# Kernel optimization log

Measured on AMD Instinct MI355X. Metric: run time of the kernel, lower is better.

The kernel has to match this reference:

```python
import jax, jax.numpy as jnp
import numpy as np

N_NODES = 100000
N_EDGES = 1600000
N_GRAPHS = 128
DIM = 128
N_LAYERS = 4
EPS = 1e-5


def setup_inputs() -> dict:
    key = jax.random.key(0)
    ks = jax.random.split(key, 8)
    h = jax.random.normal(ks[0], (N_NODES, DIM), dtype=jnp.float32)
    src = jax.random.randint(ks[1], (N_EDGES,), 0, N_NODES, dtype=jnp.int32)
    dst = jax.random.randint(ks[2], (N_EDGES,), 0, N_NODES, dtype=jnp.int32)
    graph_id = jnp.sort(jax.random.randint(ks[3], (N_NODES,), 0, N_GRAPHS, dtype=jnp.int32))
    sc = 1.0 / np.sqrt(DIM)
    W_embed = jax.random.normal(ks[4], (DIM, DIM), dtype=jnp.float32) * sc
    b_embed = jnp.zeros((DIM,), jnp.float32)
    W_layers = jax.random.normal(ks[5], (N_LAYERS, DIM, DIM), dtype=jnp.float32) * sc
    b_layers = jnp.zeros((N_LAYERS, DIM), jnp.float32)
    gamma = jnp.ones((N_LAYERS, DIM), jnp.float32)
    beta = jnp.zeros((N_LAYERS, DIM), jnp.float32)
    return {"h": h, "src": src, "dst": dst, "graph_id": graph_id,
            "W_embed": W_embed, "b_embed": b_embed, "W_layers": W_layers,
            "b_layers": b_layers, "gamma": gamma, "beta": beta}


def _gcn_forward(h, src, dst, graph_id, W_embed, b_embed, W_layers, b_layers, gamma, beta):
    # symmetric GraphConv normalization (norm='both'): D_out^{-1/2} on src, D_in^{-1/2} on dst
    ones_e = jnp.ones((src.shape[0],), h.dtype)
    deg_out = jax.ops.segment_sum(ones_e, src, num_segments=N_NODES)
    deg_in = jax.ops.segment_sum(ones_e, dst, num_segments=N_NODES)
    norm_src = jax.lax.rsqrt(jnp.maximum(deg_out, 1.0))
    norm_dst = jax.lax.rsqrt(jnp.maximum(deg_in, 1.0))

    # input embedding (dropout = identity in eval)
    h = h @ W_embed + b_embed

    for l in range(N_LAYERS):
        h_in = h
        # gather-aggregate-scatter: m_e = h_src * norm_src; sum into dst; scale by norm_dst
        m = (h * norm_src[:, None])[src]                         # [E, D]
        agg = jax.ops.segment_sum(m, dst, num_segments=N_NODES)  # [N, D]
        hl = (agg * norm_dst[:, None]) @ W_layers[l] + b_layers[l]
        # batch norm over node dimension (training-mode batch stats)
        mu = jnp.mean(hl, axis=0)
        var = jnp.var(hl, axis=0)
        hl = (hl - mu) * jax.lax.rsqrt(var + EPS) * gamma[l] + beta[l]
        hl = jax.nn.relu(hl)
        h = hl + h_in  # residual (dims match all layers)

    # mean readout per graph
    sums = jax.ops.segment_sum(h, graph_id, num_segments=N_GRAPHS)           # [G, D]
    cnts = jax.ops.segment_sum(jnp.ones((N_NODES,), h.dtype), graph_id, num_segments=N_GRAPHS)
    return sums / jnp.maximum(cnts, 1.0)[:, None]


def reference(h, src, dst, graph_id, W_embed, b_embed, W_layers, b_layers, gamma, beta):
    return _gcn_forward(h, src, dst, graph_id, W_embed, b_embed, W_layers, b_layers, gamma, beta)
```

## Files before the change

kernel.cpp:

```cpp
#include <hip/hip_runtime.h>
#include <hip/hip_bf16.h>
#include <hip/hip_fp16.h>


#define N_NODES 100000
#define N_EDGES 1600000
#define N_GRAPHS 128
#define DIM 128
#define N_LAYERS 4
#define BN_EPS 1e-5f
#define NBUCK 196
#define EPB 6250
#define SREP 64

typedef __attribute__((ext_vector_type(8))) _Float16 half8;
typedef __attribute__((ext_vector_type(4))) float floatx4;
typedef __attribute__((ext_vector_type(2))) float floatx2;

__global__ __launch_bounds__(256) void binA_k(const int* __restrict__ src,
                                              const int* __restrict__ dst,
                                              int* __restrict__ cnt_d,
                                              int* __restrict__ cnt_s,
                                              int* __restrict__ bh_d,
                                              int* __restrict__ bh_s) {
  __shared__ int hd[NBUCK], hs[NBUCK];
  int t = threadIdx.x;
  for (int i = t; i < NBUCK; i += 256) { hd[i] = 0; hs[i] = 0; }
  __syncthreads();
  int e0 = blockIdx.x * EPB;
  for (int e = e0 + t; e < e0 + EPB; e += 256) {
    atomicAdd(&hd[dst[e] >> 9], 1);
    atomicAdd(&hs[src[e] >> 9], 1);
  }
  __syncthreads();
  for (int i = t; i < NBUCK; i += 256) {
    int v = hd[i], v2 = hs[i];
    bh_d[blockIdx.x * NBUCK + i] = v;
    bh_s[blockIdx.x * NBUCK + i] = v2;
    if (v) atomicAdd(&cnt_d[i], v);
    if (v2) atomicAdd(&cnt_s[i], v2);
  }
}

__global__ __launch_bounds__(256) void scan196_k(
    const int* __restrict__ cnt_d, const int* __restrict__ cnt_s,
    int* __restrict__ base_d, int* __restrict__ cur_d,
    int* __restrict__ base_s, int* __restrict__ cur_s,
    int* __restrict__ row_start) {
  __shared__ int sd[256], ss[256];
  int t = threadIdx.x;
  int vd = (t < NBUCK) ? cnt_d[t] : 0;
  int vs = (t < NBUCK) ? cnt_s[t] : 0;
  sd[t] = vd;
  ss[t] = vs;
  __syncthreads();
  for (int off = 1; off < 256; off <<= 1) {
    int ad = (t >= off) ? sd[t - off] : 0;
    int as = (t >= off) ? ss[t - off] : 0;
    __syncthreads();
    sd[t] += ad;
    ss[t] += as;
    __syncthreads();
  }
  if (t < NBUCK) {
    base_d[t] = sd[t] - vd;
    cur_d[t] = sd[t] - vd;
    base_s[t] = ss[t] - vs;
    cur_s[t] = ss[t] - vs;
  }
  if (t == 0) {
    base_d[NBUCK] = N_EDGES;
    base_s[NBUCK] = N_EDGES;
    row_start[N_NODES] = N_EDGES;
  }
}

__global__ __launch_bounds__(256) void scat_k(
    const int* __restrict__ src, const int* __restrict__ dst,
    int* __restrict__ cur_d, int* __restrict__ cur_s,
    const int* __restrict__ bh_d, const int* __restrict__ bh_s,
    int* __restrict__ packed, unsigned short* __restrict__ locs) {
  __shared__ int hd[NBUCK], hs[NBUCK];
  int t = threadIdx.x;
  for (int i = t; i < NBUCK; i += 256) {
    hd[i] = bh_d[blockIdx.x * NBUCK + i];
    hs[i] = bh_s[blockIdx.x * NBUCK + i];
  }
  __syncthreads();
  if (t < NBUCK) {
    hd[t] = atomicAdd(&cur_d[t], hd[t]);
    hs[t] = atomicAdd(&cur_s[t], hs[t]);
  }
  __syncthreads();
  int e0 = blockIdx.x * EPB;
  for (int e = e0 + t; e < e0 + EPB; e += 256) {
    int s = src[e], d = dst[e];
    int slot = atomicAdd(&hd[d >> 9], 1);
    packed[slot] = ((d & 511) << 17) | s;
    int slot2 = atomicAdd(&hs[s >> 9], 1);
    locs[slot2] = (unsigned short)(s & 511);
  }
}

__global__ __launch_bounds__(256) void cd_k(const int* __restrict__ base_d,
                                            const int* __restrict__ packed,
                                            int* __restrict__ row_start,
                                            int* __restrict__ csr_src,
                                            float* __restrict__ norm_dst) {
  __shared__ int sdeg[512], sinc[512], scur[512];
  int t = threadIdx.x;
  int b = blockIdx.x;
  int nbase = b << 9;
  int e0 = base_d[b], e1 = base_d[b + 1];
  sdeg[t] = 0;
  sdeg[t + 256] = 0;
  __syncthreads();
  for (int e = e0 + t; e < e1; e += 256) atomicAdd(&sdeg[packed[e] >> 17], 1);
  __syncthreads();
  sinc[t] = sdeg[t];
  sinc[t + 256] = sdeg[t + 256];
  __syncthreads();
  for (int off = 1; off < 512; off <<= 1) {
    int a0 = (t >= off) ? sinc[t - off] : 0;
    int i1 = t + 256;
    int a1 = (i1 >= off) ? sinc[i1 - off] : 0;
    __syncthreads();
    sinc[t] += a0;
    sinc[i1] += a1;
    __syncthreads();
  }
#pragma unroll
  for (int half = 0; half < 2; ++half) {
    int j = t + half * 256;
    int lofs = e0 + sinc[j] - sdeg[j];
    scur[j] = lofs;
    int node = nbase + j;
    if (node < N_NODES) {
      row_start[node] = lofs;
      int d = sdeg[j];
      norm_dst[node] = rsqrtf((float)(d > 1 ? d : 1));
    }
  }
  __syncthreads();
  for (int e = e0 + t; e < e1; e += 256) {
    int p = packed[e];
    int slot = atomicAdd(&scur[p >> 17], 1);
    csr_src[slot] = p & 0x1FFFF;
  }
}

__global__ __launch_bounds__(256) void cs_k(const int* __restrict__ base_s,
                                            const unsigned short* __restrict__ locs,
                                            float* __restrict__ norm_src) {
  __shared__ int sdeg[512];
  int t = threadIdx.x;
  int b = blockIdx.x;
  int nbase = b << 9;
  int e0 = base_s[b], e1 = base_s[b + 1];
  sdeg[t] = 0;
  sdeg[t + 256] = 0;
  __syncthreads();
  for (int e = e0 + t; e < e1; e += 256) atomicAdd(&sdeg[locs[e]], 1);
  __syncthreads();
#pragma unroll
  for (int half = 0; half < 2; ++half) {
    int j = t + half * 256;
    int node = nbase + j;
    if (node < N_NODES) {
      int d = sdeg[j];
      norm_src[node] = rsqrtf((float)(d > 1 ? d : 1));
    }
  }
}

__global__ __launch_bounds__(256) void wswz_k(const float* __restrict__ W_embed,
                                              const float* __restrict__ W_layers,
                                              __half* __restrict__ Bsw) {
  int m = blockIdx.x >> 3, ct = blockIdx.x & 7;
  const float* Wm =
      (m == 0) ? W_embed : (W_layers + (size_t)(m - 1) * 16384);
  int ks = threadIdx.x >> 6, lane = threadIdx.x & 63;
  int n = ct * 16 + (lane & 15);
  int k0 = ks * 32 + (lane >> 4) * 8;
  __half* o = Bsw + ((((size_t)m * 8 + ct) * 4 + ks) * 64 + lane) * 8;
#pragma unroll
  for (int j = 0; j < 8; ++j) o[j] = __float2half(Wm[(k0 + j) * 128 + n]);
}

__device__ inline void mfma_core16(const __half* sA,
                                   const __half* __restrict__ Bsw,
                                   floatx4 (&acc)[8], int w, int lane,
                                   int quad, int lrow) {
#pragma unroll
  for (int ct = 0; ct < 8; ++ct) acc[ct] = (floatx4)(0.f);
#pragma unroll
  for (int ks = 0; ks < 4; ++ks) {
    int m = w * 16 + lrow;
    half8 afrag = *(const half8*)(&sA[m * 136 + ks * 32 + quad * 8]);
#pragma unroll
    for (int ct = 0; ct < 8; ++ct) {
      half8 bfrag = *(const half8*)(&Bsw[(((size_t)ct * 4 + ks) * 64 + lane) * 8]);
      acc[ct] = __builtin_amdgcn_mfma_f32_16x16x32_f16(afrag, bfrag, acc[ct],
                                                       0, 0, 0);
    }
  }
}

__device__ inline void accf8x16(float (&a)[16], uint4 v) {
  floatx2 f;
  f = __builtin_amdgcn_cvt_pk_f32_fp8(v.x, false); a[0] += f.x;  a[1] += f.y;
  f = __builtin_amdgcn_cvt_pk_f32_fp8(v.x, true);  a[2] += f.x;  a[3] += f.y;
  f = __builtin_amdgcn_cvt_pk_f32_fp8(v.y, false); a[4] += f.x;  a[5] += f.y;
  f = __builtin_amdgcn_cvt_pk_f32_fp8(v.y, true);  a[6] += f.x;  a[7] += f.y;
  f = __builtin_amdgcn_cvt_pk_f32_fp8(v.z, false); a[8] += f.x;  a[9] += f.y;
  f = __builtin_amdgcn_cvt_pk_f32_fp8(v.z, true);  a[10] += f.x; a[11] += f.y;
  f = __builtin_amdgcn_cvt_pk_f32_fp8(v.w, false); a[12] += f.x; a[13] += f.y;
  f = __builtin_amdgcn_cvt_pk_f32_fp8(v.w, true);  a[14] += f.x; a[15] += f.y;
}

__global__ __launch_bounds__(256) void mfma_gemm_f32in(
    const float* __restrict__ X32, const __half* __restrict__ Bsw,
    const float* __restrict__ bias, __half* __restrict__ A16,
    unsigned char* __restrict__ S8, const float* __restrict__ norm_src) {
  __shared__ __half sA[64 * 136];
  const int tid = threadIdx.x;
  const int w = tid >> 6, lane = tid & 63;
  const int quad = lane >> 4, lrow = lane & 15;
  const int row_base = blockIdx.x * 64;

#pragma unroll
  for (int i = 0; i < 8; ++i) {
    int g = i * 256 + tid;
    int r = g >> 5, q = g & 31;
    int row = row_base + r;
    float4 v = make_float4(0.f, 0.f, 0.f, 0.f);
    if (row < N_NODES) v = ((const float4*)X32)[(size_t)row * 32 + q];
    union { __half2 h[2]; float f[2]; } u;
    u.h[0] = __floats2half2_rn(v.x, v.y);
    u.h[1] = __floats2half2_rn(v.z, v.w);
    *(float2*)(&sA[r * 136 + q * 4]) = *(float2*)u.f;
  }
  __syncthreads();

  floatx4 acc[8];
  mfma_core16(sA, Bsw, acc, w, lane, quad, lrow);

  float bcol[8];
#pragma unroll
  for (int ct = 0; ct < 8; ++ct) bcol[ct] = bias[ct * 16 + lrow];

  float* sC = (float*)sA;
#pragma unroll
  for (int h = 0; h < 2; ++h) {
    __syncthreads();
    if ((w >> 1) == h) {
      int hw = w & 1;
#pragma unroll
      for (int ct = 0; ct < 8; ++ct)
#pragma unroll
        for (int reg = 0; reg < 4; ++reg)
          sC[(hw * 16 + quad * 4 + reg) * 132 + ct * 16 + lrow] =
              acc[ct][reg] + bcol[ct];
    }
    __syncthreads();
#pragma unroll
    for (int k = 0; k < 4; ++k) {
      int c = k * 256 + tid;
      int hr = c >> 5;
      int col = (c & 31) * 4;
      int row = row_base + h * 32 + hr;
      if (row < N_NODES) {
        float4 y = *(const float4*)&sC[hr * 132 + col];
        union { __half2 hh[2]; float2 f; } u;
        u.hh[0] = __floats2half2_rn(y.x, y.y);
        u.hh[1] = __floats2half2_rn(y.z, y.w);
        *(float2*)(A16 + (size_t)row * 128 + col) = u.f;
        float ns = norm_src[row];
        unsigned pb = 0;
        pb = __builtin_amdgcn_cvt_pk_fp8_f32(y.x * ns, y.y * ns, pb, false);
        pb = __builtin_amdgcn_cvt_pk_fp8_f32(y.z * ns, y.w * ns, pb, true);
        *(unsigned*)(S8 + (size_t)row * 128 + col) = pb;
      }
    }
  }
}

__global__ __launch_bounds__(256) void gag_k(
    const uint4* __restrict__ Hs, const int* __restrict__ row_start,
    const int* __restrict__ csr_src, const float* __restrict__ norm_dst,
    const __half* __restrict__ Bsw, const float* __restrict__ bias,
    __half* __restrict__ hl16, float* __restrict__ stats) {
  __shared__ __half sA[64 * 136];
  __shared__ float sred[1024];
  const int tid = threadIdx.x;
  const int w = tid >> 6, lane = tid & 63;
  const int quad = lane >> 4, lrow = lane & 15;
  const int row_base = blockIdx.x * 64;
  const int l8 = tid & 7;

#pragma unroll
  for (int pass = 0; pass < 2; ++pass) {
    int r = pass * 32 + (tid >> 3);
    int node = row_base + r;
    float a[16];
#pragma unroll
    for (int i = 0; i < 16; ++i) a[i] = 0.f;
    float nd = 0.f;
    if (node < N_NODES) {
      nd = norm_dst[node];
      int s0 = row_start[node], s1 = row_start[node + 1];
      int deg = s1 - s0;
      int full_end = s0 + (deg & ~7);
      for (int e = s0; e < full_end; e += 8) {
        int idx = csr_src[e + l8];
        uint4 v0 = Hs[(size_t)__shfl(idx, 0, 8) * 8 + l8];
        uint4 v1 = Hs[(size_t)__shfl(idx, 1, 8) * 8 + l8];
        uint4 v2 = Hs[(size_t)__shfl(idx, 2, 8) * 8 + l8];
        uint4 v3 = Hs[(size_t)__shfl(idx, 3, 8) * 8 + l8];
        uint4 v4 = Hs[(size_t)__shfl(idx, 4, 8) * 8 + l8];
        uint4 v5 = Hs[(size_t)__shfl(idx, 5, 8) * 8 + l8];
        uint4 v6 = Hs[(size_t)__shfl(idx, 6, 8) * 8 + l8];
        uint4 v7 = Hs[(size_t)__shfl(idx, 7, 8) * 8 + l8];
        accf8x16(a, v0); accf8x16(a, v1); accf8x16(a, v2); accf8x16(a, v3);
        accf8x16(a, v4); accf8x16(a, v5); accf8x16(a, v6); accf8x16(a, v7);
      }
      int cnt = s1 - full_end;
      if (cnt) {
        int idx = (l8 < cnt) ? csr_src[full_end + l8] : 0;
        int j = 0;
        for (; j + 4 <= cnt; j += 4) {
          uint4 v0 = Hs[(size_t)__shfl(idx, j, 8) * 8 + l8];
          uint4 v1 = Hs[(size_t)__shfl(idx, j + 1, 8) * 8 + l8];
          uint4 v2 = Hs[(size_t)__shfl(idx, j + 2, 8) * 8 + l8];
          uint4 v3 = Hs[(size_t)__shfl(idx, j + 3, 8) * 8 + l8];
          accf8x16(a, v0); accf8x16(a, v1); accf8x16(a, v2); accf8x16(a, v3);
        }
        for (; j < cnt; ++j) {
          accf8x16(a, Hs[(size_t)__shfl(idx, j, 8) * 8 + l8]);
        }
      }
    }
    union { __half2 hh[8]; float4 f[2]; } u;
#pragma unroll
    for (int q = 0; q < 8; ++q)
      u.hh[q] = __floats2half2_rn(a[2 * q] * nd, a[2 * q + 1] * nd);
    *(float4*)(&sA[r * 136 + l8 * 16]) = u.f[0];
    *(float4*)(&sA[r * 136 + l8 * 16 + 8]) = u.f[1];
  }
  __syncthreads();

  floatx4 acc[8];
  mfma_core16(sA, Bsw, acc, w, lane, quad, lrow);

  float bcol[8], psum[8], pqsum[8];
#pragma unroll
  for (int ct = 0; ct < 8; ++ct) {
    bcol[ct] = bias[ct * 16 + lrow];
    psum[ct] = 0.f;
    pqsum[ct] = 0.f;
#pragma unroll
    for (int reg = 0; reg < 4; ++reg) {
      int row = row_base + w * 16 + quad * 4 + reg;
      if (row < N_NODES) {
        float y = acc[ct][reg] + bcol[ct];
        psum[ct] += y;
        pqsum[ct] += y * y;
      }
    }
  }
#pragma unroll
  for (int ct = 0; ct < 8; ++ct) {
    psum[ct] += __shfl_xor(psum[ct], 16, 64);
    psum[ct] += __shfl_xor(psum[ct], 32, 64);
    pqsum[ct] += __shfl_xor(pqsum[ct], 16, 64);
    pqsum[ct] += __shfl_xor(pqsum[ct], 32, 64);
  }
  if (quad == 0) {
#pragma unroll
    for (int ct = 0; ct < 8; ++ct) {
      sred[w * 128 + ct * 16 + lrow] = psum[ct];
      sred[512 + w * 128 + ct * 16 + lrow] = pqsum[ct];
    }
  }
  __syncthreads();
  if (tid < 128) {
    float s = sred[tid] + sred[128 + tid] + sred[256 + tid] + sred[384 + tid];
    float q = sred[512 + tid] + sred[640 + tid] + sred[768 + tid] +
              sred[896 + tid];
    float* st = stats + (size_t)(blockIdx.x & (SREP - 1)) * 256;
    atomicAdd(&st[tid], s);
    atomicAdd(&st[128 + tid], q);
  }

  float* sC = (float*)sA;
#pragma unroll
  for (int h = 0; h < 2; ++h) {
    __syncthreads();
    if ((w >> 1) == h) {
      int hw = w & 1;
#pragma unroll
      for (int ct = 0; ct < 8; ++ct)
#pragma unroll
        for (int reg = 0; reg < 4; ++reg)
          sC[(hw * 16 + quad * 4 + reg) * 132 + ct * 16 + lrow] =
              acc[ct][reg] + bcol[ct];
    }
    __syncthreads();
#pragma unroll
    for (int k = 0; k < 4; ++k) {
      int c = k * 256 + tid;
      int hr = c >> 5;
      int col = (c & 31) * 4;
      int row = row_base + h * 32 + hr;
      if (row < N_NODES) {
        float4 y = *(const float4*)&sC[hr * 132 + col];
        union { __half2 hh[2]; float2 f; } u;
        u.hh[0] = __floats2half2_rn(y.x, y.y);
        u.hh[1] = __floats2half2_rn(y.z, y.w);
        *(float2*)(hl16 + (size_t)row * 128 + col) = u.f;
      }
    }
  }
}

__global__ __launch_bounds__(128) void bn_fin_k(const float* __restrict__ stats,
                                                const float* __restrict__ gamma,
                                                const float* __restrict__ beta,
                                                float* __restrict__ sc_sh) {
  int c = threadIdx.x;
  float s = 0.f, q = 0.f;
  for (int r = 0; r < SREP; ++r) {
    s += stats[r * 256 + c];
    q += stats[r * 256 + 128 + c];
  }
  const float invn = 1.0f / (float)N_NODES;
  float mean = s * invn;
  float var = q * invn - mean * mean;
  var = fmaxf(var, 0.f);
  float sc = gamma[c] * rsqrtf(var + BN_EPS);
  sc_sh[c] = sc;
  sc_sh[128 + c] = beta[c] - mean * sc;
}

__global__ __launch_bounds__(256) void bnrelu_k(
    const __half* __restrict__ hl16, __half* __restrict__ A16,
    unsigned char* __restrict__ S8, const float* __restrict__ sc_sh,
    const float* __restrict__ norm_src, int write_scaled) {
  int idx = blockIdx.x * 256 + threadIdx.x;
  int node = idx >> 4;
  int c8 = idx & 15;
  float4 hv4 = *(const float4*)(hl16 + (size_t)idx * 8);
  float4 av4 = *(const float4*)(A16 + (size_t)idx * 8);
  const __half2* hp = (const __half2*)&hv4;
  const __half2* ap = (const __half2*)&av4;
  const float4* sv = (const float4*)sc_sh;
  float4 s0 = sv[c8 * 2], s1 = sv[c8 * 2 + 1];
  float4 b0 = sv[32 + c8 * 2], b1 = sv[32 + c8 * 2 + 1];
  float n = write_scaled ? norm_src[node] : 0.f;
  float2 f0 = __half22float2(hp[0]), f1 = __half22float2(hp[1]);
  float2 f2 = __half22float2(hp[2]), f3 = __half22float2(hp[3]);
  float2 a0 = __half22float2(ap[0]), a1 = __half22float2(ap[1]);
  float2 a2 = __half22float2(ap[2]), a3 = __half22float2(ap[3]);
  float v[8];
  v[0] = fmaxf(f0.x * s0.x + b0.x, 0.f) + a0.x;
  v[1] = fmaxf(f0.y * s0.y + b0.y, 0.f) + a0.y;
  v[2] = fmaxf(f1.x * s0.z + b0.z, 0.f) + a1.x;
  v[3] = fmaxf(f1.y * s0.w + b0.w, 0.f) + a1.y;
  v[4] = fmaxf(f2.x * s1.x + b1.x, 0.f) + a2.x;
  v[5] = fmaxf(f2.y * s1.y + b1.y, 0.f) + a2.y;
  v[6] = fmaxf(f3.x * s1.z + b1.z, 0.f) + a3.x;
  v[7] = fmaxf(f3.y * s1.w + b1.w, 0.f) + a3.y;
  union { __half2 h[4]; float4 f; } ua;
#pragma unroll
  for (int q = 0; q < 4; ++q)
    ua.h[q] = __floats2half2_rn(v[2 * q], v[2 * q + 1]);
  *(float4*)(A16 + (size_t)idx * 8) = ua.f;
  if (write_scaled) {
    unsigned lo = 0, hi = 0;
    lo = __builtin_amdgcn_cvt_pk_fp8_f32(v[0] * n, v[1] * n, lo, false);
    lo = __builtin_amdgcn_cvt_pk_fp8_f32(v[2] * n, v[3] * n, lo, true);
    hi = __builtin_amdgcn_cvt_pk_fp8_f32(v[4] * n, v[5] * n, hi, false);
    hi = __builtin_amdgcn_cvt_pk_fp8_f32(v[6] * n, v[7] * n, hi, true);
    ((uint2*)S8)[idx] = make_uint2(lo, hi);
  }
}

__global__ __launch_bounds__(256) void gbounds_k(const int* __restrict__ gid,
                                                 int* __restrict__ gstart) {
  int g = threadIdx.x;
  if (g > N_GRAPHS) return;
  int lo = 0, hi = N_NODES;
  while (lo < hi) {
    int mid = (lo + hi) >> 1;
    if (gid[mid] < g) lo = mid + 1; else hi = mid;
  }
  gstart[g] = lo;
}

__global__ __launch_bounds__(128) void gsum_k(const __half* __restrict__ A16,
                                              const int* __restrict__ gid,
                                              float* gsum) {
  int c = threadIdx.x;
  int n0 = blockIdx.x * 128;
  int n1 = n0 + 128;
  if (n1 > N_NODES) n1 = N_NODES;
  int cur = gid[n0];
  float local = 0.f;
  for (int n = n0; n < n1; ++n) {
    int g = gid[n];
    if (g != cur) {
      atomicAdd(&gsum[cur * 128 + c], local);
      local = 0.f;
      cur = g;
    }
    local += __half2float(A16[(size_t)n * 128 + c]);
  }
  atomicAdd(&gsum[cur * 128 + c], local);
}

__global__ __launch_bounds__(128) void gout_k(const float* __restrict__ gsum,
                                              const int* __restrict__ gstart,
                                              float* __restrict__ out) {
  int g = blockIdx.x, c = threadIdx.x;
  float cnt = (float)(gstart[g + 1] - gstart[g]);
  if (cnt < 1.f) cnt = 1.f;
  out[g * 128 + c] = gsum[g * 128 + c] / cnt;
}

extern "C" void kernel_launch(void* const* d_in, const int* in_sizes, int n_in,
                              void* d_out, int out_size, void* d_ws,
                              size_t ws_size, hipStream_t stream) {
  const float* h = (const float*)d_in[0];
  const int* src = (const int*)d_in[1];
  const int* dst = (const int*)d_in[2];
  const int* gid = (const int*)d_in[3];
  const float* W_embed = (const float*)d_in[4];
  const float* b_embed = (const float*)d_in[5];
  const float* W_layers = (const float*)d_in[6];
  const float* b_layers = (const float*)d_in[7];
  const float* gamma = (const float*)d_in[8];
  const float* beta = (const float*)d_in[9];
  float* out = (float*)d_out;
  (void)in_sizes; (void)n_in; (void)out_size; (void)ws_size;

  char* ws = (char*)d_ws;
  size_t o = 0;
  auto alloc = [&](size_t bytes) -> char* {
    char* p = ws + o;
    o = (o + bytes + 255) & ~(size_t)255;
    return p;
  };
  int* cnt_d = (int*)alloc(NBUCK * 4);
  int* cnt_s = (int*)alloc(NBUCK * 4);
  int* base_d = (int*)alloc((NBUCK + 1) * 4);
  int* cur_d = (int*)alloc(NBUCK * 4);
  int* base_s = (int*)alloc((NBUCK + 1) * 4);
  int* cur_s = (int*)alloc(NBUCK * 4);
  int* bh_d = (int*)alloc((size_t)256 * NBUCK * 4);
  int* bh_s = (int*)alloc((size_t)256 * NBUCK * 4);
  float* norm_src = (float*)alloc(N_NODES * 4);
  float* norm_dst = (float*)alloc(N_NODES * 4);
  int* row_start = (int*)alloc((N_NODES + 1) * 4);
  int* csr_src = (int*)alloc((size_t)N_EDGES * 4);
  int* packed = (int*)alloc((size_t)N_EDGES * 4);
  unsigned short* locs = (unsigned short*)alloc((size_t)N_EDGES * 2);
  float* stats4 = (float*)alloc((size_t)N_LAYERS * SREP * 256 * 4);
  float* gsum = (float*)alloc(N_GRAPHS * 128 * 4);
  int* gstart = (int*)alloc((N_GRAPHS + 1) * 4);
  float* sc_sh = (float*)alloc(256 * 4);
  __half* Bsw = (__half*)alloc(5 * 16384 * 2);
  __half* A16 = (__half*)alloc((size_t)N_NODES * 128 * 2);
  unsigned char* P0f8 = (unsigned char*)alloc((size_t)N_NODES * 128);
  __half* H16 = (__half*)alloc((size_t)N_NODES * 128 * 2);

  hipMemsetAsync(cnt_d, 0, 2048, stream);
  hipMemsetAsync(stats4, 0, (size_t)N_LAYERS * SREP * 256 * 4 + 65536, stream);

  binA_k<<<256, 256, 0, stream>>>(src, dst, cnt_d, cnt_s, bh_d, bh_s);
  scan196_k<<<1, 256, 0, stream>>>(cnt_d, cnt_s, base_d, cur_d, base_s, cur_s,
                                   row_start);
  scat_k<<<256, 256, 0, stream>>>(src, dst, cur_d, cur_s, bh_d, bh_s, packed,
                                  locs);
  cd_k<<<NBUCK, 256, 0, stream>>>(base_d, packed, row_start, csr_src,
                                  norm_dst);
  cs_k<<<NBUCK, 256, 0, stream>>>(base_s, locs, norm_src);

  wswz_k<<<40, 256, 0, stream>>>(W_embed, W_layers, Bsw);

  mfma_gemm_f32in<<<(N_NODES + 63) / 64, 256, 0, stream>>>(
      h, Bsw, b_embed, A16, P0f8, norm_src);

  for (int l = 0; l < N_LAYERS; ++l) {
    float* stats = stats4 + (size_t)l * SREP * 256;
    gag_k<<<(N_NODES + 63) / 64, 256, 0, stream>>>(
        (const uint4*)P0f8, row_start, csr_src, norm_dst,
        Bsw + (size_t)(1 + l) * 16384, b_layers + l * DIM, H16, stats);
    bn_fin_k<<<1, 128, 0, stream>>>(stats, gamma + l * DIM, beta + l * DIM,
                                    sc_sh);
    bnrelu_k<<<(N_NODES * 16 + 255) / 256, 256, 0, stream>>>(
        H16, A16, P0f8, sc_sh, norm_src, (l < N_LAYERS - 1) ? 1 : 0);
  }

  gbounds_k<<<1, 256, 0, stream>>>(gid, gstart);
  gsum_k<<<(N_NODES + 127) / 128, 128, 0, stream>>>(A16, gid, gsum);
  gout_k<<<N_GRAPHS, 128, 0, stream>>>(gsum, gstart, out);
}
```

Measured before the change: 556.4 us.

## Split fused gather-GEMM into separate gather and fp16 GEMM kernels

The fused gather+aggregate+GEMM kernel becomes two kernels. The first is a gather kernel that uses 16 lanes per node with 8-byte loads and high occupancy (launch_bounds 256,8). The second is a standalone MFMA GEMM that reads the aggregated fp16 rows from a new intermediate buffer. This is meant to raise memory-level parallelism in the latency-bound random gather, which the fused kernel limited through its LDS and register footprint. In exchange it writes and re-reads an extra N×128 fp16 intermediate each layer and adds one kernel launch per layer.

```diff
diff --git a/kernel.cpp b/kernel.cpp
--- a/kernel.cpp
+++ b/kernel.cpp
@@ -206,16 +206,12 @@
   }
 }
 
-__device__ inline void accf8x16(float (&a)[16], uint4 v) {
+__device__ inline void accf8x8(float (&a)[8], uint2 v) {
   floatx2 f;
-  f = __builtin_amdgcn_cvt_pk_f32_fp8(v.x, false); a[0] += f.x;  a[1] += f.y;
-  f = __builtin_amdgcn_cvt_pk_f32_fp8(v.x, true);  a[2] += f.x;  a[3] += f.y;
-  f = __builtin_amdgcn_cvt_pk_f32_fp8(v.y, false); a[4] += f.x;  a[5] += f.y;
-  f = __builtin_amdgcn_cvt_pk_f32_fp8(v.y, true);  a[6] += f.x;  a[7] += f.y;
-  f = __builtin_amdgcn_cvt_pk_f32_fp8(v.z, false); a[8] += f.x;  a[9] += f.y;
-  f = __builtin_amdgcn_cvt_pk_f32_fp8(v.z, true);  a[10] += f.x; a[11] += f.y;
-  f = __builtin_amdgcn_cvt_pk_f32_fp8(v.w, false); a[12] += f.x; a[13] += f.y;
-  f = __builtin_amdgcn_cvt_pk_f32_fp8(v.w, true);  a[14] += f.x; a[15] += f.y;
+  f = __builtin_amdgcn_cvt_pk_f32_fp8(v.x, false); a[0] += f.x; a[1] += f.y;
+  f = __builtin_amdgcn_cvt_pk_f32_fp8(v.x, true);  a[2] += f.x; a[3] += f.y;
+  f = __builtin_amdgcn_cvt_pk_f32_fp8(v.y, false); a[4] += f.x; a[5] += f.y;
+  f = __builtin_amdgcn_cvt_pk_f32_fp8(v.y, true);  a[6] += f.x; a[7] += f.y;
 }
 
 __global__ __launch_bounds__(256) void mfma_gemm_f32in(
@@ -285,67 +281,75 @@
   }
 }
 
-__global__ __launch_bounds__(256) void gag_k(
-    const uint4* __restrict__ Hs, const int* __restrict__ row_start,
+__global__ __launch_bounds__(256, 8) void gather16_k(
+    const uint2* __restrict__ Hs, const int* __restrict__ row_start,
     const int* __restrict__ csr_src, const float* __restrict__ norm_dst,
-    const __half* __restrict__ Bsw, const float* __restrict__ bias,
-    __half* __restrict__ hl16, float* __restrict__ stats) {
+    __half* __restrict__ out) {
+  int node = (blockIdx.x * 256 + threadIdx.x) >> 4;
+  int l16 = threadIdx.x & 15;
+  int l8 = l16 & 7;
+  if (node >= N_NODES) return;
+  int s0 = row_start[node], s1 = row_start[node + 1];
+  float a[8];
+#pragma unroll
+  for (int i = 0; i < 8; ++i) a[i] = 0.f;
+  int deg = s1 - s0;
+  int full_end = s0 + (deg & ~7);
+  for (int e = s0; e < full_end; e += 8) {
+    int idx = csr_src[e + l8];
+    uint2 v0 = Hs[(size_t)__shfl(idx, 0, 16) * 16 + l16];
+    uint2 v1 = Hs[(size_t)__shfl(idx, 1, 16) * 16 + l16];
+    uint2 v2 = Hs[(size_t)__shfl(idx, 2, 16) * 16 + l16];
+    uint2 v3 = Hs[(size_t)__shfl(idx, 3, 16) * 16 + l16];
+    uint2 v4 = Hs[(size_t)__shfl(idx, 4, 16) * 16 + l16];
+    uint2 v5 = Hs[(size_t)__shfl(idx, 5, 16) * 16 + l16];
+    uint2 v6 = Hs[(size_t)__shfl(idx, 6, 16) * 16 + l16];
+    uint2 v7 = Hs[(size_t)__shfl(idx, 7, 16) * 16 + l16];
+    accf8x8(a, v0); accf8x8(a, v1); accf8x8(a, v2); accf8x8(a, v3);
+    accf8x8(a, v4); accf8x8(a, v5); accf8x8(a, v6); accf8x8(a, v7);
+  }
+  int cnt = s1 - full_end;
+  if (cnt) {
+    int idx = (l8 < cnt) ? csr_src[full_end + l8] : 0;
+    int j = 0;
+    for (; j + 4 <= cnt; j += 4) {
+      uint2 v0 = Hs[(size_t)__shfl(idx, j, 16) * 16 + l16];
+      uint2 v1 = Hs[(size_t)__shfl(idx, j + 1, 16) * 16 + l16];
+      uint2 v2 = Hs[(size_t)__shfl(idx, j + 2, 16) * 16 + l16];
+      uint2 v3 = Hs[(size_t)__shfl(idx, j + 3, 16) * 16 + l16];
+      accf8x8(a, v0); accf8x8(a, v1); accf8x8(a, v2); accf8x8(a, v3);
+    }
+    for (; j < cnt; ++j) {
+      accf8x8(a, Hs[(size_t)__shfl(idx, j, 16) * 16 + l16]);
+    }
+  }
+  float nd = norm_dst[node];
+  union { __half2 hh[4]; float4 f; } u;
+#pragma unroll
+  for (int q = 0; q < 4; ++q)
+    u.hh[q] = __floats2half2_rn(a[2 * q] * nd, a[2 * q + 1] * nd);
+  *(float4*)(out + (size_t)node * 128 + l16 * 8) = u.f;
+}
+
+__global__ __launch_bounds__(256) void mfma_gemm_f16(
+    const __half* __restrict__ X16, const __half* __restrict__ Bsw,
+    const float* __restrict__ bias, __half* __restrict__ hl16,
+    float* __restrict__ stats) {
   __shared__ __half sA[64 * 136];
   __shared__ float sred[1024];
   const int tid = threadIdx.x;
   const int w = tid >> 6, lane = tid & 63;
   const int quad = lane >> 4, lrow = lane & 15;
   const int row_base = blockIdx.x * 64;
-  const int l8 = tid & 7;
-
-#pragma unroll
-  for (int pass = 0; pass < 2; ++pass) {
-    int r = pass * 32 + (tid >> 3);
-    int node = row_base + r;
-    float a[16];
-#pragma unroll
-    for (int i = 0; i < 16; ++i) a[i] = 0.f;
-    float nd = 0.f;
-    if (node < N_NODES) {
-      nd = norm_dst[node];
-      int s0 = row_start[node], s1 = row_start[node + 1];
-      int deg = s1 - s0;
-      int full_end = s0 + (deg & ~7);
-      for (int e = s0; e < full_end; e += 8) {
-        int idx = csr_src[e + l8];
-        uint4 v0 = Hs[(size_t)__shfl(idx, 0, 8) * 8 + l8];
-        uint4 v1 = Hs[(size_t)__shfl(idx, 1, 8) * 8 + l8];
-        uint4 v2 = Hs[(size_t)__shfl(idx, 2, 8) * 8 + l8];
-        uint4 v3 = Hs[(size_t)__shfl(idx, 3, 8) * 8 + l8];
-        uint4 v4 = Hs[(size_t)__shfl(idx, 4, 8) * 8 + l8];
-        uint4 v5 = Hs[(size_t)__shfl(idx, 5, 8) * 8 + l8];
-        uint4 v6 = Hs[(size_t)__shfl(idx, 6, 8) * 8 + l8];
-        uint4 v7 = Hs[(size_t)__shfl(idx, 7, 8) * 8 + l8];
-        accf8x16(a, v0); accf8x16(a, v1); accf8x16(a, v2); accf8x16(a, v3);
-        accf8x16(a, v4); accf8x16(a, v5); accf8x16(a, v6); accf8x16(a, v7);
-      }
-      int cnt = s1 - full_end;
-      if (cnt) {
-        int idx = (l8 < cnt) ? csr_src[full_end + l8] : 0;
-        int j = 0;
-        for (; j + 4 <= cnt; j += 4) {
-          uint4 v0 = Hs[(size_t)__shfl(idx, j, 8) * 8 + l8];
-          uint4 v1 = Hs[(size_t)__shfl(idx, j + 1, 8) * 8 + l8];
-          uint4 v2 = Hs[(size_t)__shfl(idx, j + 2, 8) * 8 + l8];
-          uint4 v3 = Hs[(size_t)__shfl(idx, j + 3, 8) * 8 + l8];
-          accf8x16(a, v0); accf8x16(a, v1); accf8x16(a, v2); accf8x16(a, v3);
-        }
-        for (; j < cnt; ++j) {
-          accf8x16(a, Hs[(size_t)__shfl(idx, j, 8) * 8 + l8]);
-        }
-      }
-    }
-    union { __half2 hh[8]; float4 f[2]; } u;
-#pragma unroll
-    for (int q = 0; q < 8; ++q)
-      u.hh[q] = __floats2half2_rn(a[2 * q] * nd, a[2 * q + 1] * nd);
-    *(float4*)(&sA[r * 136 + l8 * 16]) = u.f[0];
-    *(float4*)(&sA[r * 136 + l8 * 16 + 8]) = u.f[1];
+
+#pragma unroll
+  for (int i = 0; i < 4; ++i) {
+    int g = i * 256 + tid;
+    int r = g >> 4, p = g & 15;
+    int row = row_base + r;
+    float4 v = make_float4(0.f, 0.f, 0.f, 0.f);
+    if (row < N_NODES) v = ((const float4*)X16)[(size_t)row * 16 + p];
+    *(float4*)(&sA[r * 136 + p * 8]) = v;
   }
   __syncthreads();
 
@@ -571,6 +575,7 @@
   __half* Bsw = (__half*)alloc(5 * 16384 * 2);
   __half* A16 = (__half*)alloc((size_t)N_NODES * 128 * 2);
   unsigned char* P0f8 = (unsigned char*)alloc((size_t)N_NODES * 128);
+  __half* P1h = (__half*)alloc((size_t)N_NODES * 128 * 2);
   __half* H16 = (__half*)alloc((size_t)N_NODES * 128 * 2);
 
   hipMemsetAsync(cnt_d, 0, 2048, stream);
@@ -592,9 +597,10 @@
 
   for (int l = 0; l < N_LAYERS; ++l) {
     float* stats = stats4 + (size_t)l * SREP * 256;
-    gag_k<<<(N_NODES + 63) / 64, 256, 0, stream>>>(
-        (const uint4*)P0f8, row_start, csr_src, norm_dst,
-        Bsw + (size_t)(1 + l) * 16384, b_layers + l * DIM, H16, stats);
+    gather16_k<<<(N_NODES * 16 + 255) / 256, 256, 0, stream>>>(
+        (const uint2*)P0f8, row_start, csr_src, norm_dst, P1h);
+    mfma_gemm_f16<<<(N_NODES + 63) / 64, 256, 0, stream>>>(
+        P1h, Bsw + (size_t)(1 + l) * 16384, b_layers + l * DIM, H16, stats);
     bn_fin_k<<<1, 128, 0, stream>>>(stats, gamma + l * DIM, beta + l * DIM,
                                     sc_sh);
     bnrelu_k<<<(N_NODES * 16 + 255) / 256, 256, 0, stream>>>(
```

Result: faster. 517.0 us (-7.1%).
